# Kernel optimization log

Hardware: AMD Instinct MI355X
Metric: run time of the kernel (lower is better)

## Reference

```python
import jax, jax.numpy as jnp
import numpy as np

K_SIZE = 5  # neighborhood window

def _extract_patches(x, k):
    # tf.image.extract_patches with stride 1, SAME (zero) padding.
    # x: [B,H,W,C] -> [B,H,W,k*k,C]
    pad = k // 2
    B, H, W, C = x.shape
    xp = jnp.pad(x, ((0, 0), (pad, pad), (pad, pad), (0, 0)))
    # fixed small k*k loop (25 shifted views), stacked along patch axis
    return jnp.stack([xp[:, i:i + H, j:j + W, :]
                      for i in range(k) for j in range(k)], axis=3)

def setup_inputs() -> dict:
    key = jax.random.key(0)
    k1, k2, k3 = jax.random.split(key, 3)
    B, H, W, C, BIN = 2, 256, 256, 32, 32
    return {
        "main": jax.random.normal(k1, (B, H, W, C), dtype=jnp.float32),
        "ref": jax.random.normal(k2, (B, H, W, C), dtype=jnp.float32),
        "ref_value": jax.random.normal(k3, (B, H, W, BIN), dtype=jnp.float32),
    }

def reference(main, ref, ref_value):
    # mode='dot': local-window dot-product attention
    ref_stacked = _extract_patches(ref, K_SIZE)          # [B,H,W,k*k,C]
    attn = jnp.einsum('bhwc,bhwkc->bhwk', main, ref_stacked)
    attn = jax.nn.softmax(attn, axis=-1)                 # [B,H,W,k*k]
    # aggregate_mode='weighted_sum'
    ref_value_stacked = _extract_patches(ref_value, K_SIZE)  # [B,H,W,k*k,bin]
    return jnp.einsum('bhwk,bhwki->bhwi', attn, ref_value_stacked)
```

## Files before the change

### kernel.cpp

```cpp
#include <hip/hip_runtime.h>


__global__ void __launch_bounds__(256)
local_attn_kernel(const float* __restrict__ main_p,
                  const float* __restrict__ ref_p,
                  const float* __restrict__ rv_p,
                  float* __restrict__ out_p)
{
    const int lane = threadIdx.x & 63;
    const int wv   = threadIdx.x >> 6;
    const int cg   = lane & 7;
    const int pw   = lane >> 3;
    const int p    = (blockIdx.x * 4 + wv) * 8 + pw;

    const int rem   = p & 65535;
    const int h     = rem >> 8;
    const int w     = rem & 255;
    const int bbase = p - rem;

    const float4* m4 = (const float4*)main_p;
    const float4* r4 = (const float4*)ref_p;
    const float4* v4 = (const float4*)rv_p;
    float4*       o4 = (float4*)out_p;

    const float4 m = m4[p * 8 + cg];

    float  sum = 0.0f;
    float4 acc = make_float4(0.f, 0.f, 0.f, 0.f);

#pragma unroll
    for (int i = 0; i < 5; ++i) {
        const int  hh   = h + i - 2;
        const bool hok  = ((unsigned)hh < 256u);
        const int  rowb = bbase + min(max(hh, 0), 255) * 256;
#pragma unroll
        for (int j = 0; j < 5; ++j) {
            const int  ww   = w + j - 2;
            const bool ok   = hok && ((unsigned)ww < 256u);
            const float msk = ok ? 1.0f : 0.0f;
            const int  np   = rowb + min(max(ww, 0), 255);
            const int  a    = np * 8 + cg;

            const float4 r = r4[a];
            float s = m.x * r.x + m.y * r.y + m.z * r.z + m.w * r.w;
            s += __shfl_xor(s, 1, 64);
            s += __shfl_xor(s, 2, 64);
            s += __shfl_xor(s, 4, 64);

            const float e = __expf(s * msk);
            sum += e;

            const float4 v = v4[a];
            const float wk = e * msk;
            acc.x += wk * v.x; acc.y += wk * v.y;
            acc.z += wk * v.z; acc.w += wk * v.w;
        }
    }

    const float inv = 1.0f / sum;
    acc.x *= inv; acc.y *= inv; acc.z *= inv; acc.w *= inv;
    o4[p * 8 + cg] = acc;
}

extern "C" void kernel_launch(void* const* d_in, const int* in_sizes, int n_in,
                              void* d_out, int out_size, void* d_ws, size_t ws_size,
                              hipStream_t stream)
{
    const float* main_p = (const float*)d_in[0];
    const float* ref_p  = (const float*)d_in[1];
    const float* rv_p   = (const float*)d_in[2];
    float*       out_p  = (float*)d_out;

    const int npix   = in_sizes[0] / 32;
    const int blocks = npix / 32;
    local_attn_kernel<<<blocks, 256, 0, stream>>>(main_p, ref_p, rv_p, out_p);
}
```

Before: 105.8 us.

## Compute four vertically stacked pixels per thread to reuse neighbor loads

Each thread now handles a column of four output pixels, sweeping eight reference rows and reusing each loaded ref/value vector across every output row whose window covers it. Blocks are remapped to 2D tiles of 32x4 pixels. This cuts global/L2 load instructions per output from 50 float4 loads to about 20. In exchange it raises register pressure with four accumulators and four main vectors, and launches a quarter as many blocks. A launch-bounds occupancy hint is also added.

Result: slower. 397.7 us (+276.0%).

```diff
diff --git a/kernel.cpp b/kernel.cpp
--- a/kernel.cpp
+++ b/kernel.cpp
@@ -1,7 +1,7 @@
 #include <hip/hip_runtime.h>
 
 
-__global__ void __launch_bounds__(256)
+__global__ void __launch_bounds__(256, 4)
 local_attn_kernel(const float* __restrict__ main_p,
                   const float* __restrict__ ref_p,
                   const float* __restrict__ rv_p,
@@ -11,55 +11,76 @@
     const int wv   = threadIdx.x >> 6;
     const int cg   = lane & 7;
     const int pw   = lane >> 3;
-    const int p    = (blockIdx.x * 4 + wv) * 8 + pw;
 
-    const int rem   = p & 65535;
-    const int h     = rem >> 8;
-    const int w     = rem & 255;
-    const int bbase = p - rem;
+    const int b     = blockIdx.x;
+    const int batch = b >> 9;
+    const int tb    = b & 511;
+    const int ty    = tb >> 3;
+    const int tx    = tb & 7;
+    const int w0    = tx * 32 + wv * 8 + pw;
+    const int h0    = ty * 4;
+    const int bbase = batch << 16;
 
     const float4* m4 = (const float4*)main_p;
     const float4* r4 = (const float4*)ref_p;
     const float4* v4 = (const float4*)rv_p;
     float4*       o4 = (float4*)out_p;
 
-    const float4 m = m4[p * 8 + cg];
+    float4 m0 = m4[(bbase + (h0 + 0) * 256 + w0) * 8 + cg];
+    float4 m1 = m4[(bbase + (h0 + 1) * 256 + w0) * 8 + cg];
+    float4 m2 = m4[(bbase + (h0 + 2) * 256 + w0) * 8 + cg];
+    float4 m3 = m4[(bbase + (h0 + 3) * 256 + w0) * 8 + cg];
 
-    float  sum = 0.0f;
-    float4 acc = make_float4(0.f, 0.f, 0.f, 0.f);
+    int   ccol[5];
+    float cmask[5];
+#pragma unroll
+    for (int dj = 0; dj < 5; ++dj) {
+        const int ww = w0 + dj - 2;
+        cmask[dj] = ((unsigned)ww < 256u) ? 1.0f : 0.0f;
+        ccol[dj]  = min(max(ww, 0), 255);
+    }
+
+    float  sum0 = 0.f, sum1 = 0.f, sum2 = 0.f, sum3 = 0.f;
+    float4 a0 = make_float4(0.f,0.f,0.f,0.f), a1 = a0, a2 = a0, a3 = a0;
 
 #pragma unroll
-    for (int i = 0; i < 5; ++i) {
-        const int  hh   = h + i - 2;
-        const bool hok  = ((unsigned)hh < 256u);
-        const int  rowb = bbase + min(max(hh, 0), 255) * 256;
+    for (int ri = 0; ri < 8; ++ri) {
+        const int   hh   = h0 + ri - 2;
+        const float rok  = ((unsigned)hh < 256u) ? 1.0f : 0.0f;
+        const int   rowb = bbase + min(max(hh, 0), 255) * 256;
 #pragma unroll
-        for (int j = 0; j < 5; ++j) {
-            const int  ww   = w + j - 2;
-            const bool ok   = hok && ((unsigned)ww < 256u);
-            const float msk = ok ? 1.0f : 0.0f;
-            const int  np   = rowb + min(max(ww, 0), 255);
-            const int  a    = np * 8 + cg;
-
-            const float4 r = r4[a];
-            float s = m.x * r.x + m.y * r.y + m.z * r.z + m.w * r.w;
-            s += __shfl_xor(s, 1, 64);
-            s += __shfl_xor(s, 2, 64);
-            s += __shfl_xor(s, 4, 64);
-
-            const float e = __expf(s * msk);
-            sum += e;
-
-            const float4 v = v4[a];
-            const float wk = e * msk;
-            acc.x += wk * v.x; acc.y += wk * v.y;
-            acc.z += wk * v.z; acc.w += wk * v.w;
+        for (int dj = 0; dj < 5; ++dj) {
+            const int   aoff = (rowb + ccol[dj]) * 8 + cg;
+            const float msk  = rok * cmask[dj];
+            const float4 r = r4[aoff];
+            const float4 v = v4[aoff];
+#pragma unroll
+            for (int t = (ri > 4 ? ri - 4 : 0); t <= (ri < 3 ? ri : 3); ++t) {
+                const float4 mt = (t == 0) ? m0 : (t == 1) ? m1 : (t == 2) ? m2 : m3;
+                float s = mt.x * r.x + mt.y * r.y + mt.z * r.z + mt.w * r.w;
+                s += __shfl_xor(s, 1, 64);
+                s += __shfl_xor(s, 2, 64);
+                s += __shfl_xor(s, 4, 64);
+                const float e  = __expf(s * msk);
+                const float wk = e * msk;
+                if (t == 0) { sum0 += e; a0.x += wk*v.x; a0.y += wk*v.y; a0.z += wk*v.z; a0.w += wk*v.w; }
+                if (t == 1) { sum1 += e; a1.x += wk*v.x; a1.y += wk*v.y; a1.z += wk*v.z; a1.w += wk*v.w; }
+                if (t == 2) { sum2 += e; a2.x += wk*v.x; a2.y += wk*v.y; a2.z += wk*v.z; a2.w += wk*v.w; }
+                if (t == 3) { sum3 += e; a3.x += wk*v.x; a3.y += wk*v.y; a3.z += wk*v.z; a3.w += wk*v.w; }
+            }
         }
     }
 
-    const float inv = 1.0f / sum;
-    acc.x *= inv; acc.y *= inv; acc.z *= inv; acc.w *= inv;
-    o4[p * 8 + cg] = acc;
+    const float i0 = 1.0f / sum0, i1 = 1.0f / sum1, i2 = 1.0f / sum2, i3 = 1.0f / sum3;
+    a0.x *= i0; a0.y *= i0; a0.z *= i0; a0.w *= i0;
+    a1.x *= i1; a1.y *= i1; a1.z *= i1; a1.w *= i1;
+    a2.x *= i2; a2.y *= i2; a2.z *= i2; a2.w *= i2;
+    a3.x *= i3; a3.y *= i3; a3.z *= i3; a3.w *= i3;
+
+    o4[(bbase + (h0 + 0) * 256 + w0) * 8 + cg] = a0;
+    o4[(bbase + (h0 + 1) * 256 + w0) * 8 + cg] = a1;
+    o4[(bbase + (h0 + 2) * 256 + w0) * 8 + cg] = a2;
+    o4[(bbase + (h0 + 3) * 256 + w0) * 8 + cg] = a3;
 }
 
 extern "C" void kernel_launch(void* const* d_in, const int* in_sizes, int n_in,
@@ -72,6 +93,6 @@
     float*       out_p  = (float*)d_out;
 
     const int npix   = in_sizes[0] / 32;
-    const int blocks = npix / 32;
+    const int blocks = npix / 128;
     local_attn_kernel<<<blocks, 256, 0, stream>>>(main_p, ref_p, rv_p, out_p);
 }
```
